# Kernel optimization log

Hardware: AMD Instinct MI355X
Metric: run time of the kernel (lower is better)

## Reference

```python
import jax, jax.numpy as jnp
import numpy as np

N_LAYERS = 4
D = 768
H = 12
DK = D // H
FF = 2048
SD = 5
DIM_LOC = 6
EPS = 1e-10


def layer_norm(x, g, b, eps=1e-5):
    m = x.mean(-1, keepdims=True)
    v = ((x - m) ** 2).mean(-1, keepdims=True)
    return (x - m) / jnp.sqrt(v + eps) * g + b


def calc_pairwise_locs(centers):
    # centers: [b, l, 3] -> [b, l, t, 5] spatial relation features ('center' type, dist-normalized)
    rel = centers[:, :, None, :] - centers[:, None, :, :]
    d = jnp.sqrt(jnp.sum(rel ** 2, -1) + EPS)
    max_d = jnp.max(d.reshape(d.shape[0], -1), -1)
    dn = d / max_d[:, None, None]
    d2 = jnp.sqrt(jnp.sum(rel[..., :2] ** 2, -1) + EPS)
    return jnp.stack([dn, rel[..., 2] / d, d2 / d, rel[..., 1] / d2, rel[..., 0] / d2], -1)


def setup_inputs() -> dict:
    key = jax.random.key(0)
    ks = jax.random.split(key, 32)
    B, L = 16, 512
    std = 0.02
    inp = {
        'obj_embeds': jax.random.normal(ks[0], (B, L, D), jnp.float32),
        'obj_locs': jax.random.uniform(ks[1], (B, L, DIM_LOC), jnp.float32) * 5.0,
        'obj_masks': jnp.ones((B, L), jnp.bool_),
        # single loc layer (obj_loc_encoding='same_all')
        'loc_w': jax.random.normal(ks[2], (DIM_LOC, D), jnp.float32) * std,
        'loc_b': jnp.zeros((D,), jnp.float32),
        'loc_ln_g': jnp.ones((D,), jnp.float32),
        'loc_ln_b': jnp.zeros((D,), jnp.float32),
        # per-layer params, stacked on leading layer dim
        'Wq': jax.random.normal(ks[3], (N_LAYERS, D, D), jnp.float32) * std,
        'bq': jnp.zeros((N_LAYERS, D), jnp.float32),
        'Wk': jax.random.normal(ks[4], (N_LAYERS, D, D), jnp.float32) * std,
        'bk': jnp.zeros((N_LAYERS, D), jnp.float32),
        'Wv': jax.random.normal(ks[5], (N_LAYERS, D, D), jnp.float32) * std,
        'bv': jnp.zeros((N_LAYERS, D), jnp.float32),
        'Wfc': jax.random.normal(ks[6], (N_LAYERS, D, D), jnp.float32) * std,
        'bfc': jnp.zeros((N_LAYERS, D), jnp.float32),
        'loc_fc_w': jax.random.normal(ks[7], (N_LAYERS, SD, H), jnp.float32) * std,
        'loc_fc_b': jnp.zeros((N_LAYERS, H), jnp.float32),
        'ln0_g': jnp.ones((N_LAYERS, D), jnp.float32),
        'ln0_b': jnp.zeros((N_LAYERS, D), jnp.float32),
        'W1': jax.random.normal(ks[8], (N_LAYERS, D, FF), jnp.float32) * std,
        'b1': jnp.zeros((N_LAYERS, FF), jnp.float32),
        'W2': jax.random.normal(ks[9], (N_LAYERS, FF, D), jnp.float32) * std,
        'b2': jnp.zeros((N_LAYERS, D), jnp.float32),
        'ln1_g': jnp.ones((N_LAYERS, D), jnp.float32),
        'ln1_b': jnp.zeros((N_LAYERS, D), jnp.float32),
        'ln2_g': jnp.ones((N_LAYERS, D), jnp.float32),
        'ln2_b': jnp.zeros((N_LAYERS, D), jnp.float32),
    }
    return inp


def _forward(obj_embeds, obj_locs, obj_masks, loc_w, loc_b, loc_ln_g, loc_ln_b,
             Wq, bq, Wk, bk, Wv, bv, Wfc, bfc, loc_fc_w, loc_fc_b, ln0_g, ln0_b,
             W1, b1, W2, b2, ln1_g, ln1_b, ln2_g, ln2_b):
    B, L, _ = obj_embeds.shape
    pl = calc_pairwise_locs(obj_locs[..., :3])        # [b,l,t,5]
    kpm = jnp.logical_not(obj_masks)                  # key_padding_mask: True = pad
    mask = kpm[:, None, None, :]                      # [b,1,1,t]
    query_pos = layer_norm(obj_locs @ loc_w + loc_b, loc_ln_g, loc_ln_b)
    x = obj_embeds
    scale = np.float32(1.0 / np.sqrt(DK))
    for i in range(N_LAYERS):
        x = x + query_pos  # obj_loc_encoding='same_all': add loc embedding every layer
        res = x
        q = (x @ Wq[i] + bq[i]).reshape(B, L, H, DK)
        k = (x @ Wk[i] + bk[i]).reshape(B, L, H, DK)
        v = (x @ Wv[i] + bv[i]).reshape(B, L, H, DK)
        attn = jnp.einsum('blhk,bthk->bhlt', q, k) * scale
        loc_attn = jax.nn.relu(jnp.einsum('bltd,dh->bhlt', pl, loc_fc_w[i])
                               + loc_fc_b[i][None, :, None, None])
        attn = jnp.where(mask, -1e30, attn)
        loc_attn = jnp.where(mask, 0.0, loc_attn)
        fused = jax.nn.softmax(jnp.log(jnp.clip(loc_attn, 1e-6)) + attn, axis=-1)
        out = jnp.einsum('bhlt,bthv->blhv', fused, v).reshape(B, L, D)
        out = out @ Wfc[i] + bfc[i]
        x2 = layer_norm(out + res, ln0_g[i], ln0_b[i])   # attn-internal residual + LN
        x = layer_norm(x + x2, ln1_g[i], ln1_b[i])       # encoder-layer norm1
        ff = jax.nn.gelu(x @ W1[i] + b1[i], approximate=False) @ W2[i] + b2[i]
        x = layer_norm(x + ff, ln2_g[i], ln2_b[i])       # encoder-layer norm2
    return x


def reference(obj_embeds, obj_locs, obj_masks, loc_w, loc_b, loc_ln_g, loc_ln_b,
              Wq, bq, Wk, bk, Wv, bv, Wfc, bfc, loc_fc_w, loc_fc_b, ln0_g, ln0_b,
              W1, b1, W2, b2, ln1_g, ln1_b, ln2_g, ln2_b):
    return _forward(obj_embeds, obj_locs, obj_masks, loc_w, loc_b, loc_ln_g, loc_ln_b,
                    Wq, bq, Wk, bk, Wv, bv, Wfc, bfc, loc_fc_w, loc_fc_b, ln0_g, ln0_b,
                    W1, b1, W2, b2, ln1_g, ln1_b, ln2_g, ln2_b)
```

## Files before the change

### kernel.cpp

```cpp
#include <hip/hip_runtime.h>
#include <hip/hip_bf16.h>
#include <math.h>

#define NL 4
#define D 768
#define H 12
#define DK 64
#define FF 2048
#define SD 5
#define DLOC 6
#define B 16
#define L 512
#define M (B*L)

typedef unsigned short u16;
typedef unsigned int u32;
typedef __attribute__((ext_vector_type(8))) __bf16 bf16x8;
typedef __attribute__((ext_vector_type(4))) float f32x4;

__device__ inline float b2f(u16 u){ u32 v = ((u32)u)<<16; return __builtin_bit_cast(float, v); }
__device__ inline u16 f2b(float f){ __hip_bfloat16 h = __float2bfloat16(f); return __builtin_bit_cast(u16, h); }

__device__ inline void gld16(const u16* g, u16* l) {
    __builtin_amdgcn_global_load_lds(
        (const __attribute__((address_space(1))) u32*)(const void*)g,
        (__attribute__((address_space(3))) u32*)(void*)l, 16, 0, 0);
}

__global__ __launch_bounds__(256) void maxd_kernel(const float* __restrict__ locs,
                                                   u32* __restrict__ maxd) {
    int b = blockIdx.x >> 5;
    int seg = blockIdx.x & 31;
    __shared__ float cx[L], cy[L], cz[L];
    for (int i = threadIdx.x; i < L; i += 256) {
        const float* p = locs + ((size_t)b*L + i)*DLOC;
        cx[i] = p[0]; cy[i] = p[1]; cz[i] = p[2];
    }
    __syncthreads();
    float mx = 0.f;
    int r0 = seg*16;
    #pragma unroll
    for (int r = 0; r < 16; ++r) {
        float px = cx[r0+r], py = cy[r0+r], pz = cz[r0+r];
        for (int c = threadIdx.x; c < L; c += 256) {
            float dx = px-cx[c], dy = py-cy[c], dz = pz-cz[c];
            mx = fmaxf(mx, dx*dx + dy*dy + dz*dz);
        }
    }
    #pragma unroll
    for (int m=1;m<64;m<<=1) mx = fmaxf(mx, __shfl_xor(mx, m));
    __shared__ float wred[4];
    if ((threadIdx.x & 63) == 0) wred[threadIdx.x >> 6] = mx;
    __syncthreads();
    if (threadIdx.x == 0) {
        float v = fmaxf(fmaxf(wred[0],wred[1]), fmaxf(wred[2],wred[3]));
        float d = sqrtf(v + 1e-10f);
        atomicMax(maxd + b, __builtin_bit_cast(u32, d));
    }
}

__global__ __launch_bounds__(256) void initq_kernel(const float* __restrict__ embeds,
    const float* __restrict__ locs, const float* __restrict__ lw, const float* __restrict__ lb,
    const float* __restrict__ lg, const float* __restrict__ lbb,
    float* __restrict__ x, u16* __restrict__ xb) {
    int row = blockIdx.x;
    float lc[DLOC];
    #pragma unroll
    for (int d=0; d<DLOC; d++) lc[d] = locs[(size_t)row*DLOC + d];
    float mv[3], s1 = 0.f, s2 = 0.f;
    #pragma unroll
    for (int e = 0; e < 3; e++) {
        int col = threadIdx.x + 256*e;
        float v = lb[col];
        #pragma unroll
        for (int d = 0; d < DLOC; d++) v += lc[d]*lw[d*D + col];
        mv[e] = v; s1 += v; s2 += v*v;
    }
    __shared__ float r1[256], r2[256];
    r1[threadIdx.x]=s1; r2[threadIdx.x]=s2; __syncthreads();
    for (int s=128;s>0;s>>=1){
        if(threadIdx.x<s){r1[threadIdx.x]+=r1[threadIdx.x+s]; r2[threadIdx.x]+=r2[threadIdx.x+s];}
        __syncthreads();
    }
    float mean = r1[0]*(1.0f/D);
    float var  = r2[0]*(1.0f/D) - mean*mean;
    float rstd = rsqrtf(var + 1e-5f);
    #pragma unroll
    for (int e=0;e<3;e++){
        int col = threadIdx.x+256*e;
        float qp = (mv[e]-mean)*rstd*lg[col]+lbb[col];
        float v = embeds[(size_t)row*D+col] + qp;
        x[(size_t)row*D+col] = v;
        xb[(size_t)row*D+col] = f2b(v);
    }
}

__global__ __launch_bounds__(256) void ln01_kernel(const float* __restrict__ t0f,
    const float* __restrict__ xin,
    const float* __restrict__ g0, const float* __restrict__ b0,
    const float* __restrict__ g1, const float* __restrict__ b1,
    float* __restrict__ xout, u16* __restrict__ xb) {
    int row = blockIdx.x;
    __shared__ float r1[256], r2[256];
    float xv[3], vv[3], s1=0.f, s2=0.f;
    #pragma unroll
    for (int e=0;e<3;e++){
        int col = threadIdx.x+256*e;
        float xr = xin[(size_t)row*D+col];
        float v = t0f[(size_t)row*D+col] + xr;
        xv[e]=xr; vv[e]=v; s1+=v; s2+=v*v;
    }
    r1[threadIdx.x]=s1; r2[threadIdx.x]=s2; __syncthreads();
    for (int s=128;s>0;s>>=1){
        if(threadIdx.x<s){r1[threadIdx.x]+=r1[threadIdx.x+s]; r2[threadIdx.x]+=r2[threadIdx.x+s];}
        __syncthreads();
    }
    float mean0 = r1[0]*(1.0f/D);
    float var0  = r2[0]*(1.0f/D) - mean0*mean0;
    float rstd0 = rsqrtf(var0 + 1e-5f);
    __syncthreads();
    float uv[3]; s1=0.f; s2=0.f;
    #pragma unroll
    for (int e=0;e<3;e++){
        int col = threadIdx.x+256*e;
        float x2 = (vv[e]-mean0)*rstd0*g0[col]+b0[col];
        float u = xv[e] + x2;
        uv[e]=u; s1+=u; s2+=u*u;
    }
    r1[threadIdx.x]=s1; r2[threadIdx.x]=s2; __syncthreads();
    for (int s=128;s>0;s>>=1){
        if(threadIdx.x<s){r1[threadIdx.x]+=r1[threadIdx.x+s]; r2[threadIdx.x]+=r2[threadIdx.x+s];}
        __syncthreads();
    }
    float mean1 = r1[0]*(1.0f/D);
    float var1  = r2[0]*(1.0f/D) - mean1*mean1;
    float rstd1 = rsqrtf(var1 + 1e-5f);
    #pragma unroll
    for (int e=0;e<3;e++){
        int col = threadIdx.x+256*e;
        float v = (uv[e]-mean1)*rstd1*g1[col]+b1[col];
        xout[(size_t)row*D+col] = v;
        xb[(size_t)row*D+col] = f2b(v);
    }
}

template<int LAST>
__global__ __launch_bounds__(256) void ln2q_kernel(const float* __restrict__ xin,
    const float* __restrict__ t0f, const float* __restrict__ g2, const float* __restrict__ b2,
    const float* __restrict__ locs, const float* __restrict__ lw, const float* __restrict__ lb,
    const float* __restrict__ lg, const float* __restrict__ lbb,
    float* __restrict__ xout, u16* __restrict__ xb) {
    int row = blockIdx.x;
    __shared__ float r1[256], r2[256], r3[256], r4[256];
    float lc[DLOC];
    if (!LAST) {
        #pragma unroll
        for (int d=0; d<DLOC; d++) lc[d] = locs[(size_t)row*DLOC + d];
    }
    float vv[3], mv[3], s1=0.f, s2=0.f, s3=0.f, s4=0.f;
    #pragma unroll
    for (int e=0;e<3;e++){
        int col = threadIdx.x+256*e;
        float v = xin[(size_t)row*D+col] + t0f[(size_t)row*D+col];
        vv[e]=v; s1+=v; s2+=v*v;
        if (!LAST) {
            float mvv = lb[col];
            #pragma unroll
            for (int d = 0; d < DLOC; d++) mvv += lc[d]*lw[d*D + col];
            mv[e]=mvv; s3+=mvv; s4+=mvv*mvv;
        }
    }
    r1[threadIdx.x]=s1; r2[threadIdx.x]=s2;
    if (!LAST) { r3[threadIdx.x]=s3; r4[threadIdx.x]=s4; }
    __syncthreads();
    for (int s=128;s>0;s>>=1){
        if(threadIdx.x<s){
            r1[threadIdx.x]+=r1[threadIdx.x+s]; r2[threadIdx.x]+=r2[threadIdx.x+s];
            if (!LAST){ r3[threadIdx.x]+=r3[threadIdx.x+s]; r4[threadIdx.x]+=r4[threadIdx.x+s]; }
        }
        __syncthreads();
    }
    float mean = r1[0]*(1.0f/D);
    float var  = r2[0]*(1.0f/D) - mean*mean;
    float rstd = rsqrtf(var + 1e-5f);
    float mean3=0.f, rstd3=0.f;
    if (!LAST) {
        mean3 = r3[0]*(1.0f/D);
        float var3 = r4[0]*(1.0f/D) - mean3*mean3;
        rstd3 = rsqrtf(var3 + 1e-5f);
    }
    #pragma unroll
    for (int e=0;e<3;e++){
        int col = threadIdx.x+256*e;
        float xn = (vv[e]-mean)*rstd*g2[col]+b2[col];
        if (LAST) {
            xout[(size_t)row*D+col] = xn;
        } else {
            float qp = (mv[e]-mean3)*rstd3*lg[col]+lbb[col];
            float v = xn + qp;
            xout[(size_t)row*D+col] = v;
            xb[(size_t)row*D+col] = f2b(v);
        }
    }
}

__global__ __launch_bounds__(256) void convT_kernel(const float* __restrict__ in,
    u16* __restrict__ out, int K, int N) {
    __shared__ float tile[32][33];
    int kb = blockIdx.y*32, nb = blockIdx.x*32;
    int tx = threadIdx.x & 31, ty = threadIdx.x >> 5;
    #pragma unroll
    for (int i=0;i<32;i+=8)
        tile[ty+i][tx] = in[(size_t)(kb+ty+i)*N + nb+tx];
    __syncthreads();
    #pragma unroll
    for (int i=0;i<32;i+=8)
        out[(size_t)(nb+ty+i)*K + kb+tx] = f2b(tile[tx][ty+i]);
}

__global__ __launch_bounds__(256) void biaspack_kernel(const float* __restrict__ bq,
    const float* __restrict__ bk, const float* __restrict__ bv, float* __restrict__ outb) {
    int i = blockIdx.x*256 + threadIdx.x;
    int l = i / (3*D), j = i % (3*D);
    float v = (j < D) ? bq[l*D + j] : (j < 2*D ? bk[l*D + j - D] : bv[l*D + j - 2*D]);
    outb[i] = v;
}

template<int OUT_BF16, int ACT>
__global__ __launch_bounds__(256) void mm_kernel(
    const u16* __restrict__ A, const u16* __restrict__ Bt,
    const float* __restrict__ bias, void* __restrict__ Cout, int K, int N)
{
    __shared__ u16 As[128*32];
    __shared__ u16 Bs[128*32];
    const int tid = threadIdx.x;
    const int lane = tid & 63, wv = tid >> 6;
    const int m0 = blockIdx.y*128, n0 = blockIdx.x*128;
    const int wm = (wv>>1)*64, wn = (wv&1)*64;

    const u16* ag = A  + (size_t)(m0 + wv*16 + (lane>>2))*K + (lane&3)*8;
    const u16* bg = Bt + (size_t)(n0 + wv*16 + (lane>>2))*K + (lane&3)*8;
    u16* al0 = As + wv*512;  u16* al1 = As + 2048 + wv*512;
    u16* bl0 = Bs + wv*512;  u16* bl1 = Bs + 2048 + wv*512;
    const size_t rstep = (size_t)64*K;

    f32x4 acc[4][4];
    #pragma unroll
    for (int i=0;i<4;i++)
        #pragma unroll
        for (int j=0;j<4;j++) acc[i][j] = (f32x4){0.f,0.f,0.f,0.f};

    const int lr = lane & 15, kq = lane >> 4;
    const u16* Arow = As + (wm + lr)*32 + kq*8;
    const u16* Brow = Bs + (wn + lr)*32 + kq*8;

    for (int k0 = 0; k0 < K; k0 += 32) {
        gld16(ag + k0, al0);
        gld16(ag + rstep + k0, al1);
        gld16(bg + k0, bl0);
        gld16(bg + rstep + k0, bl1);
        __syncthreads();
        bf16x8 af[4], bfr[4];
        #pragma unroll
        for (int i=0;i<4;i++) af[i]  = *(const bf16x8*)(Arow + i*512);
        #pragma unroll
        for (int j=0;j<4;j++) bfr[j] = *(const bf16x8*)(Brow + j*512);
        #pragma unroll
        for (int i=0;i<4;i++)
            #pragma unroll
            for (int j=0;j<4;j++)
                acc[i][j] = __builtin_amdgcn_mfma_f32_16x16x32_bf16(af[i], bfr[j], acc[i][j], 0,0,0);
        __syncthreads();
    }

    const int cr = (lane>>4)*4, cc = lane & 15;
    #pragma unroll
    for (int i=0;i<4;i++) {
        int row = m0 + wm + i*16 + cr;
        #pragma unroll
        for (int j=0;j<4;j++) {
            int col = n0 + wn + j*16 + cc;
            float bv_ = bias[col];
            #pragma unroll
            for (int r=0;r<4;r++) {
                float v = acc[i][j][r] + bv_;
                if (ACT) v = 0.5f*v*(1.0f + erff(v*0.70710678f));
                if (OUT_BF16) ((u16*)Cout)[(size_t)(row+r)*N + col] = f2b(v);
                else        ((float*)Cout)[(size_t)(row+r)*N + col] = v;
            }
        }
    }
}

__global__ __launch_bounds__(256) void attn_kernel(
    const u16* __restrict__ qkv, const float* __restrict__ locs,
    const float* __restrict__ maxdp, const float* __restrict__ lfw,
    const float* __restrict__ lfb, u16* __restrict__ out)
{
    const int RS = 3*D;
    const float SC = 0.18033688f;
    const int bid = blockIdx.x;
    const int qt = bid & 7;
    const int hp = (bid >> 3) % 6;
    const int b  = bid / 48;
    const int qb = qt*64;
    const int h0 = hp*2;

    __shared__ u16 Ks[2][64*64];
    __shared__ u16 Vt[2][64*64];
    __shared__ u16 Pl[2][4*16*64];
    __shared__ float Cts[64][4];

    const int t = threadIdx.x;
    const int lane = t & 63, wv = t >> 6;
    const int l15 = lane & 15, l4 = lane >> 4;

    bf16x8 qf[2][2];
    {
        const u16* qr = qkv + (size_t)(b*L + qb + wv*16 + l15)*RS + h0*DK + l4*8;
        qf[0][0] = *(const bf16x8*)(qr);
        qf[0][1] = *(const bf16x8*)(qr + 32);
        qf[1][0] = *(const bf16x8*)(qr + DK);
        qf[1][1] = *(const bf16x8*)(qr + DK + 32);
    }
    float cqx[4], cqy[4], cqz[4];
    #pragma unroll
    for (int r=0;r<4;r++){
        const float* p = locs + (size_t)(b*L + qb + wv*16 + l4*4 + r)*DLOC;
        cqx[r]=p[0]; cqy[r]=p[1]; cqz[r]=p[2];
    }
    const float invmd = 1.0f / maxdp[b];
    float w0p[2], w1[2], w2[2], w3[2], w4[2], wbb[2];
    #pragma unroll
    for (int hh=0; hh<2; hh++){
        int h = h0+hh;
        w0p[hh] = lfw[0*H+h]*invmd; w1[hh]=lfw[1*H+h]; w2[hh]=lfw[2*H+h];
        w3[hh]=lfw[3*H+h]; w4[hh]=lfw[4*H+h]; wbb[hh]=lfb[h];
    }

    f32x4 oacc[2][4];
    float mrun[2][4], lrun[2][4];
    #pragma unroll
    for (int hh=0;hh<2;hh++)
        #pragma unroll
        for (int j=0;j<4;j++){ oacc[hh][j] = (f32x4){0.f,0.f,0.f,0.f};
                               mrun[hh][j] = -1e30f; lrun[hh][j] = 0.f; }

    const int srow0 = (wv*64 + lane) >> 3;
    const int sslot = lane & 7;

    for (int kt = 0; kt < L; kt += 64) {
        const u16* kgb = qkv + (size_t)(b*L + kt)*RS + D + h0*DK;
        {
            int r0 = srow0, r1 = srow0 + 32;
            int c0 = (sslot ^ (r0&7))*8, c1 = (sslot ^ (r1&7))*8;
            gld16(kgb + (size_t)r0*RS + c0, &Ks[0][wv*512]);
            gld16(kgb + (size_t)r1*RS + c1, &Ks[0][2048 + wv*512]);
            gld16(kgb + DK + (size_t)r0*RS + c0, &Ks[1][wv*512]);
            gld16(kgb + DK + (size_t)r1*RS + c1, &Ks[1][2048 + wv*512]);
        }
        #pragma unroll
        for (int hh=0; hh<2; hh++){
            const u16* vp = qkv + (size_t)(b*L + kt + lane)*RS + 2*D + (h0+hh)*DK + wv*16;
            bf16x8 v0 = *(const bf16x8*)(vp);
            bf16x8 v1 = *(const bf16x8*)(vp + 8);
            int d0 = wv*16;
            #pragma unroll
            for (int e=0;e<8;e++){
                Vt[hh][(d0+e)*64   + (lane ^ (e<<3))] = ((const u16*)&v0)[e];
                Vt[hh][(d0+8+e)*64 + (lane ^ (e<<3))] = ((const u16*)&v1)[e];
            }
        }
        if (t < 64) {
            #pragma unroll
            for (int d=0;d<3;d++) Cts[t][d] = locs[(size_t)(b*L + kt + t)*DLOC + d];
        }
        __syncthreads();

        f32x4 sacc[2][4];
        #pragma unroll
        for (int hh=0;hh<2;hh++)
            #pragma unroll
            for (int j=0;j<4;j++){
                sacc[hh][j] = (f32x4){0.f,0.f,0.f,0.f};
                #pragma unroll
                for (int c=0;c<2;c++){
                    int row = j*16 + l15;
                    int slot = l4 + 4*c;
                    bf16x8 kf = *(const bf16x8*)(&Ks[hh][row*64 + ((slot ^ (row&7))*8)]);
                    sacc[hh][j] = __builtin_amdgcn_mfma_f32_16x16x32_bf16(qf[hh][c], kf, sacc[hh][j], 0,0,0);
                }
            }

        float ctx[4], cty[4], ctz[4];
        #pragma unroll
        for (int j=0;j<4;j++){
            int c = l15 + 16*j;
            ctx[j]=Cts[c][0]; cty[j]=Cts[c][1]; ctz[j]=Cts[c][2];
        }

        float alr[2][4];
        #pragma unroll
        for (int r=0;r<4;r++){
            float f0[4], f1[4], f2[4], f3[4], f4[4];
            #pragma unroll
            for (int j=0;j<4;j++){
                float rx = cqx[r]-ctx[j], ry = cqy[r]-cty[j], rz = cqz[r]-ctz[j];
                float d2e = fmaf(ry,ry, fmaf(rx,rx, 1e-10f));
                float r2  = fmaf(rz,rz, d2e);
                float invd  = __builtin_amdgcn_rsqf(r2);
                float invd2 = __builtin_amdgcn_rsqf(d2e);
                f0[j] = r2*invd;
                f1[j] = rz*invd;
                f2[j] = (d2e*invd2)*invd;
                f3[j] = ry*invd2;
                f4[j] = rx*invd2;
            }
            #pragma unroll
            for (int hh=0; hh<2; hh++){
                float sv[4], la[4];
                #pragma unroll
                for (int j=0;j<4;j++){
                    float z = fmaf(f0[j], w0p[hh],
                              fmaf(f1[j], w1[hh],
                              fmaf(f2[j], w2[hh],
                              fmaf(f3[j], w3[hh],
                              fmaf(f4[j], w4[hh], wbb[hh])))));
                    la[j] = fmaxf(z, 1e-6f);
                    sv[j] = sacc[hh][j][r]*SC;
                }
                float mx = fmaxf(fmaxf(sv[0],sv[1]), fmaxf(sv[2],sv[3]));
                #pragma unroll
                for (int msk=1; msk<16; msk<<=1) mx = fmaxf(mx, __shfl_xor(mx, msk));
                float mo = mrun[hh][r];
                float mn = fmaxf(mo, mx);
                float al = __builtin_amdgcn_exp2f(mo - mn);
                float sp = 0.f;
                u16* pw = &Pl[hh][wv*1024];
                int q = l4*4 + r, sw = (q&7)<<3;
                #pragma unroll
                for (int j=0;j<4;j++){
                    float p = la[j] * __builtin_amdgcn_exp2f(sv[j] - mn);
                    sp += p;
                    pw[q*64 + ((l15 + 16*j) ^ sw)] = f2b(p);
                }
                #pragma unroll
                for (int msk=1; msk<16; msk<<=1) sp += __shfl_xor(sp, msk);
                mrun[hh][r] = mn;
                lrun[hh][r] = lrun[hh][r]*al + sp;
                alr[hh][r] = al;
            }
        }

        #pragma unroll
        for (int hh=0; hh<2; hh++){
            #pragma unroll
            for (int j=0;j<4;j++)
                #pragma unroll
                for (int r=0;r<4;r++) oacc[hh][j][r] *= alr[hh][r];
            const u16* pr = &Pl[hh][wv*1024];
            #pragma unroll
            for (int c=0;c<2;c++){
                int prow = l15;
                int pslot = l4 + 4*c;
                bf16x8 pf = *(const bf16x8*)(pr + prow*64 + ((pslot ^ (prow&7))*8));
                #pragma unroll
                for (int j=0;j<4;j++){
                    int vrow = j*16 + l15;
                    int vslot = l4 + 4*c;
                    bf16x8 vf = *(const bf16x8*)(&Vt[hh][vrow*64 + ((vslot ^ (vrow&7))*8)]);
                    oacc[hh][j] = __builtin_amdgcn_mfma_f32_16x16x32_bf16(pf, vf, oacc[hh][j], 0,0,0);
                }
            }
        }
        __syncthreads();
    }

    #pragma unroll
    for (int hh=0; hh<2; hh++)
        #pragma unroll
        for (int r=0;r<4;r++){
            float inv = __builtin_amdgcn_rcpf(lrun[hh][r]);
            size_t obase = (size_t)(b*L + qb + wv*16 + l4*4 + r)*D + (h0+hh)*DK;
            #pragma unroll
            for (int j=0;j<4;j++)
                out[obase + l15 + 16*j] = f2b(oacc[hh][j][r] * inv);
        }
}

extern "C" void kernel_launch(void* const* d_in, const int* in_sizes, int n_in,
                              void* d_out, int out_size, void* d_ws, size_t ws_size,
                              hipStream_t stream) {
    const float* obj_embeds = (const float*)d_in[0];
    const float* obj_locs   = (const float*)d_in[1];
    const float* loc_w   = (const float*)d_in[3];
    const float* loc_b   = (const float*)d_in[4];
    const float* loc_ln_g= (const float*)d_in[5];
    const float* loc_ln_b= (const float*)d_in[6];
    const float* Wq = (const float*)d_in[7];
    const float* bq = (const float*)d_in[8];
    const float* Wk = (const float*)d_in[9];
    const float* bk = (const float*)d_in[10];
    const float* Wv = (const float*)d_in[11];
    const float* bv = (const float*)d_in[12];
    const float* Wfc= (const float*)d_in[13];
    const float* bfc= (const float*)d_in[14];
    const float* lfw= (const float*)d_in[15];
    const float* lfb= (const float*)d_in[16];
    const float* ln0_g = (const float*)d_in[17];
    const float* ln0_b = (const float*)d_in[18];
    const float* W1 = (const float*)d_in[19];
    const float* b1 = (const float*)d_in[20];
    const float* W2 = (const float*)d_in[21];
    const float* b2 = (const float*)d_in[22];
    const float* ln1_g = (const float*)d_in[23];
    const float* ln1_b = (const float*)d_in[24];
    const float* ln2_g = (const float*)d_in[25];
    const float* ln2_b = (const float*)d_in[26];

    float* x  = (float*)d_out;
    char* base = (char*)d_ws;
    u16*   xb    = (u16*)  (base);
    u16*   qkv   = (u16*)  (base + 12582912);
    u16*   aob   = (u16*)  (base + 50331648);
    float* t0f   = (float*)(base + 62914560);
    u16*   wq_t  = (u16*)  (base + 88080384);
    u16*   wfc_t = (u16*)  (base + 91619328);
    u16*   w1_t  = (u16*)  (base + 92798976);
    u16*   w2_t  = (u16*)  (base + 95944704);
    float* bqkv  = (float*)(base + 99090432);
    u32*   maxd  = (u32*)  (base + 99127296);
    u16*   h1b   = qkv;

    hipMemsetAsync(maxd, 0, B*sizeof(u32), stream);
    maxd_kernel<<<B*32, 256, 0, stream>>>(obj_locs, maxd);
    biaspack_kernel<<<(NL*3*D)/256, 256, 0, stream>>>(bq, bk, bv, bqkv);
    initq_kernel<<<M, 256, 0, stream>>>(obj_embeds, obj_locs, loc_w, loc_b,
                                        loc_ln_g, loc_ln_b, x, xb);

    for (int i = 0; i < NL; i++) {
        const size_t wo = (size_t)i*D*D;
        convT_kernel<<<dim3(24,24), 256, 0, stream>>>(Wq + wo, wq_t,             D, D);
        convT_kernel<<<dim3(24,24), 256, 0, stream>>>(Wk + wo, wq_t + D*D,       D, D);
        convT_kernel<<<dim3(24,24), 256, 0, stream>>>(Wv + wo, wq_t + 2*D*D,     D, D);
        convT_kernel<<<dim3(24,24), 256, 0, stream>>>(Wfc + wo, wfc_t,           D, D);
        convT_kernel<<<dim3(64,24), 256, 0, stream>>>(W1 + (size_t)i*D*FF, w1_t, D, FF);
        convT_kernel<<<dim3(24,64), 256, 0, stream>>>(W2 + (size_t)i*FF*D, w2_t, FF, D);

        mm_kernel<1,0><<<dim3(18,64), 256, 0, stream>>>(xb, wq_t, bqkv + i*3*D, qkv, D, 3*D);
        attn_kernel<<<B*6*8, 256, 0, stream>>>(qkv, obj_locs, (const float*)maxd,
                                               lfw + i*SD*H, lfb + i*H, aob);
        mm_kernel<0,0><<<dim3(6,64), 256, 0, stream>>>(aob, wfc_t, bfc + i*D, t0f, D, D);
        ln01_kernel<<<M, 256, 0, stream>>>(t0f, x, ln0_g + i*D, ln0_b + i*D,
                                           ln1_g + i*D, ln1_b + i*D, x, xb);
        mm_kernel<1,1><<<dim3(16,64), 256, 0, stream>>>(xb, w1_t, b1 + i*FF, h1b, D, FF);
        mm_kernel<0,0><<<dim3(6,64), 256, 0, stream>>>(h1b, w2_t, b2 + i*D, t0f, FF, D);
        if (i < NL-1)
            ln2q_kernel<0><<<M, 256, 0, stream>>>(x, t0f, ln2_g + i*D, ln2_b + i*D,
                obj_locs, loc_w, loc_b, loc_ln_g, loc_ln_b, x, xb);
        else
            ln2q_kernel<1><<<M, 256, 0, stream>>>(x, t0f, ln2_g + i*D, ln2_b + i*D,
                obj_locs, loc_w, loc_b, loc_ln_g, loc_ln_b, x, xb);
    }
}
```

Before: 1.286 ms.

## Double-buffer GEMM LDS tiles, prefetch attention K/V into registers, merge weight transposes

```diff
diff --git a/kernel.cpp b/kernel.cpp
--- a/kernel.cpp
+++ b/kernel.cpp
@@ -204,18 +204,38 @@
     }
 }
 
-__global__ __launch_bounds__(256) void convT_kernel(const float* __restrict__ in,
-    u16* __restrict__ out, int K, int N) {
+__global__ __launch_bounds__(256) void convT6_kernel(
+    const float* __restrict__ Wq, const float* __restrict__ Wk,
+    const float* __restrict__ Wv, const float* __restrict__ Wfc,
+    const float* __restrict__ W1, const float* __restrict__ W2,
+    u16* __restrict__ wq_t, u16* __restrict__ wfc_t,
+    u16* __restrict__ w1_t, u16* __restrict__ w2_t) {
+    int bid = blockIdx.x;
+    const float* in; u16* outp; int K, N, nb, kb;
+    if (bid < 1728) {
+        int m = bid / 576, r = bid % 576;
+        in = (m==0) ? Wq : (m==1) ? Wk : Wv;
+        outp = wq_t + m*D*D; K = D; N = D; nb = r % 24; kb = r / 24;
+    } else if (bid < 2304) {
+        int r = bid - 1728;
+        in = Wfc; outp = wfc_t; K = D; N = D; nb = r % 24; kb = r / 24;
+    } else if (bid < 3840) {
+        int r = bid - 2304;
+        in = W1; outp = w1_t; K = D; N = FF; nb = r % 64; kb = r / 64;
+    } else {
+        int r = bid - 3840;
+        in = W2; outp = w2_t; K = FF; N = D; nb = r % 24; kb = r / 24;
+    }
     __shared__ float tile[32][33];
-    int kb = blockIdx.y*32, nb = blockIdx.x*32;
+    int kbb = kb*32, nbb = nb*32;
     int tx = threadIdx.x & 31, ty = threadIdx.x >> 5;
     #pragma unroll
     for (int i=0;i<32;i+=8)
-        tile[ty+i][tx] = in[(size_t)(kb+ty+i)*N + nb+tx];
+        tile[ty+i][tx] = in[(size_t)(kbb+ty+i)*N + nbb+tx];
     __syncthreads();
     #pragma unroll
     for (int i=0;i<32;i+=8)
-        out[(size_t)(nb+ty+i)*K + kb+tx] = f2b(tile[tx][ty+i]);
+        outp[(size_t)(nbb+ty+i)*K + kbb+tx] = f2b(tile[tx][ty+i]);
 }
 
 __global__ __launch_bounds__(256) void biaspack_kernel(const float* __restrict__ bq,
@@ -231,8 +251,8 @@
     const u16* __restrict__ A, const u16* __restrict__ Bt,
     const float* __restrict__ bias, void* __restrict__ Cout, int K, int N)
 {
-    __shared__ u16 As[128*32];
-    __shared__ u16 Bs[128*32];
+    __shared__ u16 As[2][128*32];
+    __shared__ u16 Bs[2][128*32];
     const int tid = threadIdx.x;
     const int lane = tid & 63, wv = tid >> 6;
     const int m0 = blockIdx.y*128, n0 = blockIdx.x*128;
@@ -240,9 +260,8 @@
 
     const u16* ag = A  + (size_t)(m0 + wv*16 + (lane>>2))*K + (lane&3)*8;
     const u16* bg = Bt + (size_t)(n0 + wv*16 + (lane>>2))*K + (lane&3)*8;
-    u16* al0 = As + wv*512;  u16* al1 = As + 2048 + wv*512;
-    u16* bl0 = Bs + wv*512;  u16* bl1 = Bs + 2048 + wv*512;
     const size_t rstep = (size_t)64*K;
+    const int lofs = wv*512;
 
     f32x4 acc[4][4];
     #pragma unroll
@@ -251,15 +270,24 @@
         for (int j=0;j<4;j++) acc[i][j] = (f32x4){0.f,0.f,0.f,0.f};
 
     const int lr = lane & 15, kq = lane >> 4;
-    const u16* Arow = As + (wm + lr)*32 + kq*8;
-    const u16* Brow = Bs + (wn + lr)*32 + kq*8;
-
+
+    gld16(ag, &As[0][lofs]);
+    gld16(ag + rstep, &As[0][2048+lofs]);
+    gld16(bg, &Bs[0][lofs]);
+    gld16(bg + rstep, &Bs[0][2048+lofs]);
+    __syncthreads();
+
+    int cur = 0;
     for (int k0 = 0; k0 < K; k0 += 32) {
-        gld16(ag + k0, al0);
-        gld16(ag + rstep + k0, al1);
-        gld16(bg + k0, bl0);
-        gld16(bg + rstep + k0, bl1);
-        __syncthreads();
+        if (k0 + 32 < K) {
+            int nx = cur ^ 1, kn = k0 + 32;
+            gld16(ag + kn, &As[nx][lofs]);
+            gld16(ag + rstep + kn, &As[nx][2048+lofs]);
+            gld16(bg + kn, &Bs[nx][lofs]);
+            gld16(bg + rstep + kn, &Bs[nx][2048+lofs]);
+        }
+        const u16* Arow = &As[cur][(wm + lr)*32 + kq*8];
+        const u16* Brow = &Bs[cur][(wn + lr)*32 + kq*8];
         bf16x8 af[4], bfr[4];
         #pragma unroll
         for (int i=0;i<4;i++) af[i]  = *(const bf16x8*)(Arow + i*512);
@@ -271,6 +299,7 @@
             for (int j=0;j<4;j++)
                 acc[i][j] = __builtin_amdgcn_mfma_f32_16x16x32_bf16(af[i], bfr[j], acc[i][j], 0,0,0);
         __syncthreads();
+        cur ^= 1;
     }
 
     const int cr = (lane>>4)*4, cc = lane & 15;
@@ -346,36 +375,65 @@
         for (int j=0;j<4;j++){ oacc[hh][j] = (f32x4){0.f,0.f,0.f,0.f};
                                mrun[hh][j] = -1e30f; lrun[hh][j] = 0.f; }
 
-    const int srow0 = (wv*64 + lane) >> 3;
+    const int r0s = (wv*64 + lane) >> 3;
     const int sslot = lane & 7;
 
+    bf16x8 kreg[4];
+    bf16x8 vreg[2][2];
+    float ctr0=0.f, ctr1=0.f, ctr2=0.f;
+
+    {
+        const u16* kgb = qkv + (size_t)(b*L + 0)*RS + D + h0*DK;
+        kreg[0] = *(const bf16x8*)(kgb + (size_t)r0s*RS + sslot*8);
+        kreg[1] = *(const bf16x8*)(kgb + (size_t)(r0s+32)*RS + sslot*8);
+        kreg[2] = *(const bf16x8*)(kgb + DK + (size_t)r0s*RS + sslot*8);
+        kreg[3] = *(const bf16x8*)(kgb + DK + (size_t)(r0s+32)*RS + sslot*8);
+        const u16* vp = qkv + (size_t)(b*L + 0 + lane)*RS + 2*D + h0*DK + wv*16;
+        vreg[0][0] = *(const bf16x8*)(vp);
+        vreg[0][1] = *(const bf16x8*)(vp + 8);
+        vreg[1][0] = *(const bf16x8*)(vp + DK);
+        vreg[1][1] = *(const bf16x8*)(vp + DK + 8);
+        if (t < 64) {
+            const float* p = locs + (size_t)(b*L + 0 + t)*DLOC;
+            ctr0=p[0]; ctr1=p[1]; ctr2=p[2];
+        }
+    }
+
     for (int kt = 0; kt < L; kt += 64) {
-        const u16* kgb = qkv + (size_t)(b*L + kt)*RS + D + h0*DK;
         {
-            int r0 = srow0, r1 = srow0 + 32;
-            int c0 = (sslot ^ (r0&7))*8, c1 = (sslot ^ (r1&7))*8;
-            gld16(kgb + (size_t)r0*RS + c0, &Ks[0][wv*512]);
-            gld16(kgb + (size_t)r1*RS + c1, &Ks[0][2048 + wv*512]);
-            gld16(kgb + DK + (size_t)r0*RS + c0, &Ks[1][wv*512]);
-            gld16(kgb + DK + (size_t)r1*RS + c1, &Ks[1][2048 + wv*512]);
-        }
-        #pragma unroll
-        for (int hh=0; hh<2; hh++){
-            const u16* vp = qkv + (size_t)(b*L + kt + lane)*RS + 2*D + (h0+hh)*DK + wv*16;
-            bf16x8 v0 = *(const bf16x8*)(vp);
-            bf16x8 v1 = *(const bf16x8*)(vp + 8);
+            int c0 = (sslot ^ (r0s & 7))*8;
+            *(bf16x8*)(&Ks[0][r0s*64 + c0]) = kreg[0];
+            *(bf16x8*)(&Ks[0][(r0s+32)*64 + c0]) = kreg[1];
+            *(bf16x8*)(&Ks[1][r0s*64 + c0]) = kreg[2];
+            *(bf16x8*)(&Ks[1][(r0s+32)*64 + c0]) = kreg[3];
             int d0 = wv*16;
             #pragma unroll
-            for (int e=0;e<8;e++){
-                Vt[hh][(d0+e)*64   + (lane ^ (e<<3))] = ((const u16*)&v0)[e];
-                Vt[hh][(d0+8+e)*64 + (lane ^ (e<<3))] = ((const u16*)&v1)[e];
+            for (int hh=0; hh<2; hh++)
+                #pragma unroll
+                for (int e=0;e<8;e++){
+                    Vt[hh][(d0+e)*64   + (lane ^ (e<<3))] = ((const u16*)&vreg[hh][0])[e];
+                    Vt[hh][(d0+8+e)*64 + (lane ^ (e<<3))] = ((const u16*)&vreg[hh][1])[e];
+                }
+            if (t < 64) { Cts[t][0]=ctr0; Cts[t][1]=ctr1; Cts[t][2]=ctr2; }
+        }
+        __syncthreads();
+
+        if (kt + 64 < L) {
+            const u16* kgb = qkv + (size_t)(b*L + kt + 64)*RS + D + h0*DK;
+            kreg[0] = *(const bf16x8*)(kgb + (size_t)r0s*RS + sslot*8);
+            kreg[1] = *(const bf16x8*)(kgb + (size_t)(r0s+32)*RS + sslot*8);
+            kreg[2] = *(const bf16x8*)(kgb + DK + (size_t)r0s*RS + sslot*8);
+            kreg[3] = *(const bf16x8*)(kgb + DK + (size_t)(r0s+32)*RS + sslot*8);
+            const u16* vp = qkv + (size_t)(b*L + kt + 64 + lane)*RS + 2*D + h0*DK + wv*16;
+            vreg[0][0] = *(const bf16x8*)(vp);
+            vreg[0][1] = *(const bf16x8*)(vp + 8);
+            vreg[1][0] = *(const bf16x8*)(vp + DK);
+            vreg[1][1] = *(const bf16x8*)(vp + DK + 8);
+            if (t < 64) {
+                const float* p = locs + (size_t)(b*L + kt + 64 + t)*DLOC;
+                ctr0=p[0]; ctr1=p[1]; ctr2=p[2];
             }
         }
-        if (t < 64) {
-            #pragma unroll
-            for (int d=0;d<3;d++) Cts[t][d] = locs[(size_t)(b*L + kt + t)*DLOC + d];
-        }
-        __syncthreads();
 
         f32x4 sacc[2][4];
         #pragma unroll
@@ -540,12 +598,9 @@
 
     for (int i = 0; i < NL; i++) {
         const size_t wo = (size_t)i*D*D;
-        convT_kernel<<<dim3(24,24), 256, 0, stream>>>(Wq + wo, wq_t,             D, D);
-        convT_kernel<<<dim3(24,24), 256, 0, stream>>>(Wk + wo, wq_t + D*D,       D, D);
-        convT_kernel<<<dim3(24,24), 256, 0, stream>>>(Wv + wo, wq_t + 2*D*D,     D, D);
-        convT_kernel<<<dim3(24,24), 256, 0, stream>>>(Wfc + wo, wfc_t,           D, D);
-        convT_kernel<<<dim3(64,24), 256, 0, stream>>>(W1 + (size_t)i*D*FF, w1_t, D, FF);
-        convT_kernel<<<dim3(24,64), 256, 0, stream>>>(W2 + (size_t)i*FF*D, w2_t, FF, D);
+        convT6_kernel<<<5376, 256, 0, stream>>>(Wq + wo, Wk + wo, Wv + wo, Wfc + wo,
+                                                W1 + (size_t)i*D*FF, W2 + (size_t)i*FF*D,
+                                                wq_t, wfc_t, w1_t, w2_t);
 
         mm_kernel<1,0><<<dim3(18,64), 256, 0, stream>>>(xb, wq_t, bqkv + i*3*D, qkv, D, 3*D);
         attn_kernel<<<B*6*8, 256, 0, stream>>>(qkv, obj_locs, (const float*)maxd,
```

Measured after the change: 1.353 ms. 5.3% more time.
